# Optimization experiments

Hardware: AMD Instinct MI355X
Metric: run time of the kernel (lower is better)

Reference implementation:

```python
import jax, jax.numpy as jnp
import numpy as np

# HGT meta: 2 node types (A=0, B=1), 3 relations (src_type, dst_type)
L, T, R = 3, 2, 3
H, D = 1, 64            # PyG HGTConv default heads=1, head_dim = hidden/heads
F = H * D               # hidden_channels = input feature dim = 64
NA = NB = 131072
E = 1_000_000
REL = [(0, 1), (1, 0), (0, 0)]


def setup_inputs() -> dict:
    key = jax.random.key(0)
    ks = jax.random.split(key, 16)
    sc = 1.0 / np.sqrt(F)
    inp = {}
    inp["xA"] = jax.random.normal(ks[0], (NA, F), jnp.float32)
    inp["xB"] = jax.random.normal(ks[1], (NB, F), jnp.float32)
    # K/Q/V projections per (layer, node_type)
    inp["Wk"] = jax.random.normal(ks[2], (L, T, F, F), jnp.float32) * sc
    inp["bk"] = jnp.zeros((L, T, F), jnp.float32)
    inp["Wq"] = jax.random.normal(ks[3], (L, T, F, F), jnp.float32) * sc
    inp["bq"] = jnp.zeros((L, T, F), jnp.float32)
    inp["Wv"] = jax.random.normal(ks[4], (L, T, F, F), jnp.float32) * sc
    inp["bv"] = jnp.zeros((L, T, F), jnp.float32)
    # per (layer, relation, head) attention / message matrices and priority
    inp["a_rel"] = jax.random.normal(ks[5], (L, R, H, D, D), jnp.float32) * sc
    inp["m_rel"] = jax.random.normal(ks[6], (L, R, H, D, D), jnp.float32) * sc
    inp["p_rel"] = jnp.ones((L, R, H), jnp.float32)
    # output projection + skip gate per (layer, node_type)
    inp["Wa"] = jax.random.normal(ks[7], (L, T, F, F), jnp.float32) * sc
    inp["ba"] = jnp.zeros((L, T, F), jnp.float32)
    inp["skip"] = jnp.ones((L, T), jnp.float32)
    # final readout Linear(hidden, 1)
    inp["lin_w"] = jax.random.normal(ks[8], (F, 1), jnp.float32) * sc
    inp["lin_b"] = jnp.zeros((1,), jnp.float32)
    # edge indices: ei[0]=src, ei[1]=dst (NA == NB so one range works)
    inp["ei1"] = jax.random.randint(ks[9], (2, E), 0, NA, jnp.int32)   # A -> B
    inp["ei2"] = jax.random.randint(ks[10], (2, E), 0, NA, jnp.int32)  # B -> A
    inp["ei3"] = jax.random.randint(ks[11], (2, E), 0, NA, jnp.int32)  # A -> A
    return inp


def _hgt_layer(xs, eis, Wk, bk, Wq, bq, Wv, bv, a_rel, m_rel, p_rel, Wa, ba, skip):
    # per-type K/Q/V projections, reshaped to [N, H, D]
    k = [(xs[t] @ Wk[t] + bk[t]).reshape(-1, H, D) for t in range(T)]
    q = [(xs[t] @ Wq[t] + bq[t]).reshape(-1, H, D) for t in range(T)]
    v = [(xs[t] @ Wv[t] + bv[t]).reshape(-1, H, D) for t in range(T)]
    agg = [jnp.zeros((xs[t].shape[0], H, D), xs[t].dtype) for t in range(T)]
    inv_sqrt_d = jnp.asarray(1.0 / np.sqrt(D), xs[0].dtype)
    for r, (s, d) in enumerate(REL):
        src, dst = eis[r][0], eis[r][1]
        n_d = xs[d].shape[0]
        # relation-specific transforms on source nodes, then edge gather
        k_r = jnp.einsum('nhd,hde->nhe', k[s], a_rel[r])
        v_r = jnp.einsum('nhd,hde->nhe', v[s], m_rel[r])
        # attention score per edge per head: (q_dst . k_src) * p_rel / sqrt(D)
        score = jnp.einsum('ehd,ehd->eh', q[d][dst], k_r[src]) * p_rel[r] * inv_sqrt_d
        # segment softmax over incoming edges of each dst node (per edge type)
        mx = jax.ops.segment_max(score, dst, num_segments=n_d)
        ex = jnp.exp(score - mx[dst])
        den = jax.ops.segment_sum(ex, dst, num_segments=n_d)
        alpha = ex / den[dst]                      # [E, H]
        msg = alpha[:, :, None] * v_r[src]         # [E, H, D]
        agg[d] = agg[d] + jax.ops.segment_sum(msg, dst, num_segments=n_d)
    outs = []
    for t in range(T):
        o = jax.nn.gelu(agg[t].reshape(-1, F), approximate=False) @ Wa[t] + ba[t]
        a = jax.nn.sigmoid(skip[t])               # skip gate (out_dim == in_dim)
        outs.append(a * o + (1.0 - a) * xs[t])
    return outs


def reference(xA, xB, Wk, bk, Wq, bq, Wv, bv, a_rel, m_rel, p_rel, Wa, ba, skip,
              lin_w, lin_b, ei1, ei2, ei3):
    xs = [xA, xB]
    eis = [ei1, ei2, ei3]
    for l in range(L):
        xs = _hgt_layer(xs, eis, Wk[l], bk[l], Wq[l], bq[l], Wv[l], bv[l],
                        a_rel[l], m_rel[l], p_rel[l], Wa[l], ba[l], skip[l])
    x = jnp.concatenate(xs, axis=0)               # concat all node types
    pooled = jnp.sum(x, axis=0, keepdims=True)    # global_add_pool, batch=None
    return pooled @ lin_w + lin_b                 # Linear(hidden, 1) -> [1, 1]
```

## Files before the change

kernel.cpp:

```cpp
#include <hip/hip_runtime.h>
#include <cmath>

#define DEV __device__ __forceinline__

typedef __attribute__((ext_vector_type(8))) short short8v;
typedef __attribute__((ext_vector_type(4))) float f32x4;

DEV float atomicAddF(float* p, float v) {
    return unsafeAtomicAdd(p, v);
}

DEV float gelu_exact(float v) {
    return 0.5f * v * (1.f + erff(v * 0.70710678118654752f));
}

DEV unsigned short f32_to_bf16(float f) {
    union { float f; unsigned int u; } x; x.f = f;
    unsigned int r = x.u + 0x7fffu + ((x.u >> 16) & 1u);
    return (unsigned short)(r >> 16);
}

DEV unsigned int f4_to_fp8x4(float a, float b, float c, float d) {
    int r = __builtin_amdgcn_cvt_pk_fp8_f32(a, b, 0, false);
    r = __builtin_amdgcn_cvt_pk_fp8_f32(c, d, r, true);
    return (unsigned int)r;
}

DEV float4 fp8x4_to_f4(unsigned int w) {
    auto lo = __builtin_amdgcn_cvt_pk_f32_fp8(w, false);
    auto hi = __builtin_amdgcn_cvt_pk_f32_fp8(w, true);
    return make_float4(lo[0], lo[1], hi[0], hi[1]);
}

DEV short8v cvt8_bf16(float4 f0, float4 f1) {
    union { unsigned int u[4]; short8v s; } r;
    asm("v_cvt_pk_bf16_f32 %0, %1, %2" : "=v"(r.u[0]) : "v"(f0.x), "v"(f0.y));
    asm("v_cvt_pk_bf16_f32 %0, %1, %2" : "=v"(r.u[1]) : "v"(f0.z), "v"(f0.w));
    asm("v_cvt_pk_bf16_f32 %0, %1, %2" : "=v"(r.u[2]) : "v"(f1.x), "v"(f1.y));
    asm("v_cvt_pk_bf16_f32 %0, %1, %2" : "=v"(r.u[3]) : "v"(f1.z), "v"(f1.w));
    return r.s;
}


struct MatSetB {
    const unsigned short* Wt[3];
    const float* b[3];
    float*       y[3];
    int          mode[3];
    int          n;
};

#define BCAP2 6144
#define SB_TILE 4096
#define PSTR 129

__global__ __launch_bounds__(256) void combine_w_bf16(
    const float* __restrict__ Wk, const float* __restrict__ bk,
    const float* __restrict__ Wv, const float* __restrict__ bv,
    const float* __restrict__ a_rel, const float* __restrict__ m_rel,
    const float* __restrict__ p_rel, unsigned short* __restrict__ CWt,
    float* __restrict__ Cb)
{
    const int r = blockIdx.x, kv = blockIdx.y, l = blockIdx.z;
    const int srcT[3] = {0, 1, 0};
    const int s = srcT[r];
    const float* Wsrc = (kv == 0 ? Wk : Wv) + ((size_t)(l*2 + s)) * 4096;
    const float* bsrc = (kv == 0 ? bk : bv) + ((size_t)(l*2 + s)) * 64;
    const float* A    = (kv == 0 ? a_rel : m_rel) + ((size_t)(l*3 + r)) * 4096;
    const float scale = (kv == 0) ? p_rel[l*3 + r] * 0.125f : 1.f;

    __shared__ float Ws[4096];
    __shared__ float As[4096];
    const int tid = threadIdx.x;
    for (int k = tid; k < 4096; k += 256) { Ws[k] = Wsrc[k]; As[k] = A[k]; }
    __syncthreads();

    unsigned short* out = CWt + ((size_t)(l*6 + r*2 + kv)) * 4096;
    const int j = tid & 63;
    #pragma unroll
    for (int i = 0; i < 16; i++) {
        const int f = (tid >> 6) * 16 + i;
        float acc = 0.f;
        #pragma unroll
        for (int e = 0; e < 64; e++) acc = fmaf(Ws[f*64 + e], As[e*64 + j], acc);
        const int so = (l == 0) ? f : (4*(f & 15) + (f >> 4));
        out[j*64 + so] = f32_to_bf16(acc * scale);
    }
    if (tid < 64) {
        float acc = 0.f;
        for (int e = 0; e < 64; e++) acc = fmaf(bsrc[e], As[e*64 + tid], acc);
        Cb[(size_t)(l*6 + r*2 + kv) * 64 + tid] = acc * scale;
    }
}

__global__ __launch_bounds__(256) void prep_wt(
    const float* __restrict__ Wq, const float* __restrict__ Wa,
    unsigned short* __restrict__ Wqt, unsigned short* __restrict__ Wat)
{
    const int bid = blockIdx.x;
    const float* src; unsigned short* dst; int useSigma;
    if (bid < 6) { src = Wq + (size_t)bid * 4096; dst = Wqt + (size_t)bid * 4096;
                   useSigma = (bid >= 2); }
    else         { src = Wa + (size_t)(bid - 6) * 4096; dst = Wat + (size_t)(bid - 6) * 4096;
                   useSigma = 1; }
    for (int idx = threadIdx.x; idx < 4096; idx += 256) {
        const int c = idx >> 6, s = idx & 63;
        const int k = useSigma ? (16*(s & 3) + (s >> 2)) : s;
        dst[c*64 + s] = f32_to_bf16(src[k*64 + c]);
    }
}

__global__ __launch_bounds__(256) void proj_mfma(const float* __restrict__ x, MatSetB ms)
{
    const int tid = threadIdx.x;
    const int wv  = tid >> 6;
    const int ln  = tid & 63;
    const int j   = ln & 15;
    const int g   = ln >> 4;
    const long long rowb = (long long)blockIdx.x * 128 + wv * 32;

    short8v A[2][2];
    #pragma unroll
    for (int rg = 0; rg < 2; rg++) {
        const float* xp = x + (rowb + rg*16 + j) * 64 + g*8;
        #pragma unroll
        for (int ks = 0; ks < 2; ks++) {
            const float4 f0 = *(const float4*)(xp + ks*32);
            const float4 f1 = *(const float4*)(xp + ks*32 + 4);
            A[rg][ks] = cvt8_bf16(f0, f1);
        }
    }

    unsigned int kst[2][4];
    for (int m = 0; m < ms.n; m++) {
        short8v B[4][2];
        #pragma unroll
        for (int ct = 0; ct < 4; ct++) {
            const unsigned short* wp = ms.Wt[m] + (ct*16 + j) * 64 + g*8;
            B[ct][0] = *(const short8v*)(wp);
            B[ct][1] = *(const short8v*)(wp + 32);
        }
        f32x4 acc[2][4];
        #pragma unroll
        for (int ct = 0; ct < 4; ct++) {
            const float bm = ms.b[m][ct*16 + j];
            f32x4 bi = {bm, bm, bm, bm};
            acc[0][ct] = bi; acc[1][ct] = bi;
        }
        #pragma unroll
        for (int rg = 0; rg < 2; rg++)
            #pragma unroll
            for (int ct = 0; ct < 4; ct++) {
                acc[rg][ct] = __builtin_amdgcn_mfma_f32_16x16x32_bf16(
                    A[rg][0], B[ct][0], acc[rg][ct], 0, 0, 0);
                acc[rg][ct] = __builtin_amdgcn_mfma_f32_16x16x32_bf16(
                    A[rg][1], B[ct][1], acc[rg][ct], 0, 0, 0);
            }
        const int mode = ms.mode[m];
        if (mode == 0) {
            float* yb = ms.y[m];
            #pragma unroll
            for (int rg = 0; rg < 2; rg++)
                #pragma unroll
                for (int i = 0; i < 4; i++) {
                    const long long node = rowb + rg*16 + g*4 + i;
                    *(float4*)(yb + node*64 + j*4) = make_float4(
                        acc[rg][0][i], acc[rg][1][i], acc[rg][2][i], acc[rg][3][i]);
                }
        } else if (mode == 1) {
            #pragma unroll
            for (int rg = 0; rg < 2; rg++)
                #pragma unroll
                for (int i = 0; i < 4; i++)
                    kst[rg][i] = f4_to_fp8x4(
                        acc[rg][0][i], acc[rg][1][i], acc[rg][2][i], acc[rg][3][i]);
        } else {
            unsigned char* yb = (unsigned char*)ms.y[m];
            #pragma unroll
            for (int rg = 0; rg < 2; rg++)
                #pragma unroll
                for (int i = 0; i < 4; i++) {
                    const long long node = rowb + rg*16 + g*4 + i;
                    uint2 s;
                    s.x = kst[rg][i];
                    s.y = f4_to_fp8x4(
                        acc[rg][0][i], acc[rg][1][i], acc[rg][2][i], acc[rg][3][i]);
                    *(uint2*)(yb + node*128 + j*8) = s;
                }
        }
    }
}

__global__ __launch_bounds__(256) void scatter_bucket(
    const int* __restrict__ ei, int E, int nbuck,
    int* __restrict__ bcur, int2* __restrict__ pairbuf)
{
    __shared__ int  hist[256];
    __shared__ int  lbase[256];
    __shared__ int  gbase[256];
    __shared__ int  lcur[256];
    __shared__ int  scanbuf[256];
    __shared__ int2 stage[SB_TILE];
    const int tid = threadIdx.x;
    const int tile0 = blockIdx.x * SB_TILE;

    int2 my[16]; int mb[16];
    #pragma unroll
    for (int i = 0; i < 16; i++) {
        const int e = tile0 + tid + i*256;
        if (e < E) { my[i].x = ei[e]; my[i].y = ei[E + e]; mb[i] = my[i].y >> 9; }
        else mb[i] = -1;
    }
    hist[tid] = 0;
    __syncthreads();
    #pragma unroll
    for (int i = 0; i < 16; i++) if (mb[i] >= 0) atomicAdd(&hist[mb[i]], 1);
    __syncthreads();
    const int c = hist[tid];
    scanbuf[tid] = c;
    __syncthreads();
    for (int off = 1; off < 256; off <<= 1) {
        int add = (tid >= off) ? scanbuf[tid - off] : 0;
        __syncthreads();
        scanbuf[tid] += add;
        __syncthreads();
    }
    lbase[tid] = scanbuf[tid] - c;
    lcur[tid]  = scanbuf[tid] - c;
    if (c > 0 && tid < nbuck) gbase[tid] = atomicAdd(bcur + tid * 16, c);
    __syncthreads();
    #pragma unroll
    for (int i = 0; i < 16; i++) {
        if (mb[i] >= 0) {
            const int p = atomicAdd(&lcur[mb[i]], 1);
            stage[p] = my[i];
        }
    }
    __syncthreads();
    if (c > 0 && tid < nbuck) {
        const int gb = gbase[tid];
        const int lb = lbase[tid];
        int2* dstp = pairbuf + (size_t)tid * BCAP2;
        for (int jj = 0; jj < c; jj++) {
            const int gp = gb + jj;
            if (gp < BCAP2) dstp[gp] = stage[lb + jj];
        }
    }
}

__global__ __launch_bounds__(256) void bucket_csr(
    const int2* __restrict__ pairbuf, const int* __restrict__ bcur,
    int* __restrict__ row_ptr, int* __restrict__ row_end,
    int* __restrict__ col, int n)
{
    const int b   = blockIdx.x;
    const int tid = threadIdx.x;
    __shared__ int lcnt[512];
    __shared__ int lcur[512];
    __shared__ int scanbuf[256];
    int cnt = bcur[b * 16];
    if (cnt > BCAP2) cnt = BCAP2;
    lcnt[tid] = 0; lcnt[tid + 256] = 0;
    __syncthreads();
    const int2* src = pairbuf + (size_t)b * BCAP2;
    for (int i = tid; i < cnt; i += 256)
        atomicAdd(&lcnt[src[i].y & 511], 1);
    __syncthreads();
    const int c0 = lcnt[2*tid], c1 = lcnt[2*tid + 1];
    const int s = c0 + c1;
    scanbuf[tid] = s;
    __syncthreads();
    for (int off = 1; off < 256; off <<= 1) {
        int add = (tid >= off) ? scanbuf[tid - off] : 0;
        __syncthreads();
        scanbuf[tid] += add;
        __syncthreads();
    }
    const int excl = scanbuf[tid] - s;
    const int base = b * BCAP2;
    const int d0 = (b << 9) + 2*tid;
    if (d0 < n)     { row_ptr[d0]   = base + excl;      row_end[d0]   = base + excl + c0; }
    if (d0 + 1 < n) { row_ptr[d0+1] = base + excl + c0; row_end[d0+1] = base + excl + c0 + c1; }
    lcur[2*tid] = excl; lcur[2*tid + 1] = excl + c0;
    __syncthreads();
    for (int i = tid; i < cnt; i += 256) {
        const int2 p = src[i];
        const int pos = atomicAdd(&lcur[p.y & 511], 1);
        col[base + pos] = p.x;
    }
}

#define AGG_BODY(RP, RE, COL, KV, O0, O1)                                              \
    {                                                                                  \
        float4 acc0 = {0.f,0.f,0.f,0.f}, acc1 = {0.f,0.f,0.f,0.f};                     \
        float ssum = 0.f;                                                              \
        const int s0 = RP[dst], s1 = RE[dst];                                          \
        int src_cur = (s0 < s1) ? COL[s0] : 0;                                         \
        uint4 kvr = *(const uint4*)(KV + (size_t)src_cur * 128 + sub*16);              \
        for (int e = s0; e < s1; e++) {                                                \
            const int src_next = (e + 1 < s1) ? COL[e + 1] : 0;                        \
            const uint4 kvn = *(const uint4*)(KV + (size_t)src_next * 128 + sub*16);   \
            const float4 kA = fp8x4_to_f4(kvr.x);                                      \
            const float4 kB = fp8x4_to_f4(kvr.z);                                      \
            float sc = q0.x*kA.x + q0.y*kA.y + q0.z*kA.z + q0.w*kA.w                   \
                     + q1.x*kB.x + q1.y*kB.y + q1.z*kB.z + q1.w*kB.w;                  \
            sc += __shfl_xor(sc, 1); sc += __shfl_xor(sc, 2); sc += __shfl_xor(sc, 4); \
            const float p = __expf(sc);                                                \
            const float4 vA = fp8x4_to_f4(kvr.y);                                      \
            const float4 vB = fp8x4_to_f4(kvr.w);                                      \
            ssum += p;                                                                 \
            acc0.x = fmaf(p, vA.x, acc0.x); acc0.y = fmaf(p, vA.y, acc0.y);            \
            acc0.z = fmaf(p, vA.z, acc0.z); acc0.w = fmaf(p, vA.w, acc0.w);            \
            acc1.x = fmaf(p, vB.x, acc1.x); acc1.y = fmaf(p, vB.y, acc1.y);            \
            acc1.z = fmaf(p, vB.z, acc1.z); acc1.w = fmaf(p, vB.w, acc1.w);            \
            kvr = kvn;                                                                 \
        }                                                                              \
        const float inv = (ssum > 0.f) ? 1.f / ssum : 0.f;                             \
        O0.x = fmaf(acc0.x, inv, O0.x); O0.y = fmaf(acc0.y, inv, O0.y);                \
        O0.z = fmaf(acc0.z, inv, O0.z); O0.w = fmaf(acc0.w, inv, O0.w);                \
        O1.x = fmaf(acc1.x, inv, O1.x); O1.y = fmaf(acc1.y, inv, O1.y);                \
        O1.z = fmaf(acc1.z, inv, O1.z); O1.w = fmaf(acc1.w, inv, O1.w);                \
    }

__global__ __launch_bounds__(1024, 8) void agg_epilogue(
    const int* __restrict__ rp1, const int* __restrict__ re1, const int* __restrict__ c1,
    const int* __restrict__ rp2, const int* __restrict__ re2, const int* __restrict__ c2,
    const float* __restrict__ q,
    const unsigned char* __restrict__ kva, const unsigned char* __restrict__ kvb,
    float* __restrict__ xio, const unsigned short* __restrict__ Wat,
    const float* __restrict__ ba, const float* __restrict__ skipw,
    int xstd, int dual, int dopool, float* __restrict__ vec)
{
    __shared__ float lds[64 * PSTR];
    __shared__ float lds_pool[64];
    const int tid = threadIdx.x;
    const long long rowb = (long long)blockIdx.x * 128;
    if (tid < 64) lds_pool[tid] = 0.f;

    {
        const int sub = tid & 7;
        const int dl  = tid >> 3;
        const int dst = (int)rowb + dl;
        const float4* qp = (const float4*)(q + (size_t)dst * 64);
        const float4 q0 = qp[sub*2], q1 = qp[sub*2 + 1];
        float4 o0 = {0.f,0.f,0.f,0.f}, o1 = {0.f,0.f,0.f,0.f};
        AGG_BODY(rp1, re1, c1, kva, o0, o1)
        if (dual) {
            AGG_BODY(rp2, re2, c2, kvb, o0, o1)
        }
        float* lp = lds + (size_t)(8*sub) * PSTR + dl;
        lp[0*PSTR] = gelu_exact(o0.x); lp[1*PSTR] = gelu_exact(o0.y);
        lp[2*PSTR] = gelu_exact(o0.z); lp[3*PSTR] = gelu_exact(o0.w);
        lp[4*PSTR] = gelu_exact(o1.x); lp[5*PSTR] = gelu_exact(o1.y);
        lp[6*PSTR] = gelu_exact(o1.z); lp[7*PSTR] = gelu_exact(o1.w);
    }
    __syncthreads();

    if (tid < 512) {
        const int wv = tid >> 6;
        const int ln = tid & 63;
        const int j  = ln & 15;
        const int g  = ln >> 4;
        const int r  = wv*16 + j;

        short8v A[2];
        #pragma unroll
        for (int ks = 0; ks < 2; ks++) {
            const int pb = g*8 + ks*32;
            const float4 f0 = make_float4(lds[(pb+0)*PSTR + r], lds[(pb+1)*PSTR + r],
                                          lds[(pb+2)*PSTR + r], lds[(pb+3)*PSTR + r]);
            const float4 f1 = make_float4(lds[(pb+4)*PSTR + r], lds[(pb+5)*PSTR + r],
                                          lds[(pb+6)*PSTR + r], lds[(pb+7)*PSTR + r]);
            A[ks] = cvt8_bf16(f0, f1);
        }

        f32x4 acc[4];
        #pragma unroll
        for (int ct = 0; ct < 4; ct++) {
            const float bm = ba[ct*16 + j];
            acc[ct] = (f32x4){bm, bm, bm, bm};
        }
        #pragma unroll
        for (int ct = 0; ct < 4; ct++) {
            const unsigned short* wp = Wat + (ct*16 + j) * 64 + g*8;
            const short8v B0 = *(const short8v*)(wp);
            const short8v B1 = *(const short8v*)(wp + 32);
            acc[ct] = __builtin_amdgcn_mfma_f32_16x16x32_bf16(A[0], B0, acc[ct], 0, 0, 0);
            acc[ct] = __builtin_amdgcn_mfma_f32_16x16x32_bf16(A[1], B1, acc[ct], 0, 0, 0);
        }

        const float gate = 1.f / (1.f + __expf(-skipw[0]));
        const float og   = 1.f - gate;
        float4 pacc = {0.f,0.f,0.f,0.f};
        #pragma unroll
        for (int i = 0; i < 4; i++) {
            const long long node = rowb + wv*16 + g*4 + i;
            float* xp = xio + node*64;
            float4 o;
            if (xstd) {
                o.x = gate*acc[0][i] + og*xp[j];
                o.y = gate*acc[1][i] + og*xp[16 + j];
                o.z = gate*acc[2][i] + og*xp[32 + j];
                o.w = gate*acc[3][i] + og*xp[48 + j];
            } else {
                const float4 xo = *(const float4*)(xp + 4*j);
                o = make_float4(gate*acc[0][i] + og*xo.x,
                                gate*acc[1][i] + og*xo.y,
                                gate*acc[2][i] + og*xo.z,
                                gate*acc[3][i] + og*xo.w);
            }
            if (!dopool) {
                *(float4*)(xp + 4*j) = o;
            } else {
                pacc.x += o.x; pacc.y += o.y; pacc.z += o.z; pacc.w += o.w;
            }
        }
        if (dopool) {
            atomicAdd(&lds_pool[4*j + 0], pacc.x);
            atomicAdd(&lds_pool[4*j + 1], pacc.y);
            atomicAdd(&lds_pool[4*j + 2], pacc.z);
            atomicAdd(&lds_pool[4*j + 3], pacc.w);
        }
    }
    __syncthreads();
    if (dopool && tid < 64) atomicAddF(vec + tid, lds_pool[tid]);
}

__global__ void final_dot(const float* __restrict__ vec, const float* __restrict__ lw,
                          const float* __restrict__ lb, float* __restrict__ out)
{
    const int i = threadIdx.x;
    float v = vec[i] * lw[16*(i & 3) + (i >> 2)];
    #pragma unroll
    for (int m = 32; m >= 1; m >>= 1) v += __shfl_xor(v, m);
    if (i == 0) out[0] = v + lb[0];
}

extern "C" void kernel_launch(void* const* d_in, const int* in_sizes, int n_in,
                              void* d_out, int out_size, void* d_ws, size_t ws_size,
                              hipStream_t stream)
{
    float* xs[2] = {(float*)d_in[0], (float*)d_in[1]};
    const float* Wk    = (const float*)d_in[2];
    const float* bk    = (const float*)d_in[3];
    const float* Wq    = (const float*)d_in[4];
    const float* bq    = (const float*)d_in[5];
    const float* Wv    = (const float*)d_in[6];
    const float* bv    = (const float*)d_in[7];
    const float* a_rel = (const float*)d_in[8];
    const float* m_rel = (const float*)d_in[9];
    const float* p_rel = (const float*)d_in[10];
    const float* Wa    = (const float*)d_in[11];
    const float* ba    = (const float*)d_in[12];
    const float* skipw = (const float*)d_in[13];
    const float* lin_w = (const float*)d_in[14];
    const float* lin_b = (const float*)d_in[15];
    const int*   ei[3] = {(const int*)d_in[16], (const int*)d_in[17], (const int*)d_in[18]};

    const long long NA = in_sizes[0] / 64;
    const long long NB = in_sizes[1] / 64;
    const long long Ns[2] = {NA, NB};
    const long long Nmax = NA > NB ? NA : NB;
    int E[3];
    for (int r = 0; r < 3; r++) E[r] = in_sizes[16 + r] / 2;
    static const int dstN_is_B[3] = {1, 0, 0};
    const long long nbuckMax = (Nmax + 511) >> 9;

    float* w = (float*)d_ws;
    float* qbuf  = w; w += Nmax * 64;
    unsigned char* kv0 = (unsigned char*)w; w += Nmax * 32;
    unsigned char* kv1 = (unsigned char*)w; w += Nmax * 32;
    unsigned short* CWt = (unsigned short*)w; w += 18 * 2048;
    unsigned short* Wqt = (unsigned short*)w; w += 6 * 2048;
    unsigned short* Wat = (unsigned short*)w; w += 6 * 2048;
    float* Cb    = w; w += 18 * 64;
    float* vec   = w; w += 64;
    int* iw = (int*)w;
    int* row_ptr[3]; int* row_end[3]; int* col[3];
    for (int r = 0; r < 3; r++) {
        row_ptr[r] = iw; iw += Nmax;
        row_end[r] = iw; iw += Nmax;
        col[r]     = iw; iw += nbuckMax * BCAP2;
    }
    int*  bcur    = iw; iw += nbuckMax * 16;
    int2* pairbuf = (int2*)iw;

    combine_w_bf16<<<dim3(3, 2, 3), 256, 0, stream>>>(Wk, bk, Wv, bv, a_rel, m_rel, p_rel, CWt, Cb);
    prep_wt<<<12, 256, 0, stream>>>(Wq, Wa, Wqt, Wat);
    hipMemsetAsync(vec, 0, 64 * sizeof(float), stream);

    for (int r = 0; r < 3; r++) {
        const int n = (int)Ns[dstN_is_B[r]];
        const int nbuck = (n + 511) >> 9;
        hipMemsetAsync(bcur, 0, (size_t)nbuck * 16 * sizeof(int), stream);
        scatter_bucket<<<(E[r] + SB_TILE - 1) / SB_TILE, 256, 0, stream>>>(
            ei[r], E[r], nbuck, bcur, pairbuf);
        bucket_csr<<<nbuck, 256, 0, stream>>>(pairbuf, bcur, row_ptr[r], row_end[r], col[r], n);
    }

    const int gA = (int)(NA >> 7), gB = (int)(NB >> 7);
    for (int l = 0; l < 3; l++) {
        const int xstd   = (l == 0) ? 1 : 0;
        const int dopool = (l == 2) ? 1 : 0;
        {
            MatSetB ms; ms.n = 3;
            ms.Wt[0] = Wqt + (size_t)(l*2 + 1) * 4096;  ms.b[0] = bq + (size_t)(l*2 + 1) * 64;
            ms.y[0] = qbuf;        ms.mode[0] = 0;
            ms.Wt[1] = CWt + (size_t)(l*6 + 2) * 4096;  ms.b[1] = Cb + (size_t)(l*6 + 2) * 64;
            ms.y[1] = nullptr;     ms.mode[1] = 1;
            ms.Wt[2] = CWt + (size_t)(l*6 + 3) * 4096;  ms.b[2] = Cb + (size_t)(l*6 + 3) * 64;
            ms.y[2] = (float*)kv1; ms.mode[2] = 2;
            proj_mfma<<<gB, 256, 0, stream>>>(xs[1], ms);
        }
        {
            MatSetB ms; ms.n = 2;
            ms.Wt[0] = CWt + (size_t)(l*6 + 0) * 4096;  ms.b[0] = Cb + (size_t)(l*6 + 0) * 64;
            ms.y[0] = nullptr;     ms.mode[0] = 1;
            ms.Wt[1] = CWt + (size_t)(l*6 + 1) * 4096;  ms.b[1] = Cb + (size_t)(l*6 + 1) * 64;
            ms.y[1] = (float*)kv0; ms.mode[1] = 2;
            ms.Wt[2] = ms.Wt[1]; ms.b[2] = ms.b[1]; ms.y[2] = ms.y[1]; ms.mode[2] = 2;
            proj_mfma<<<gA, 256, 0, stream>>>(xs[0], ms);
        }
        agg_epilogue<<<gB, 1024, 0, stream>>>(
            row_ptr[0], row_end[0], col[0],
            row_ptr[0], row_end[0], col[0],
            qbuf, kv0, kv0, xs[1],
            Wat + (size_t)(l*2 + 1) * 4096, ba + (size_t)(l*2 + 1) * 64,
            skipw + l*2 + 1, xstd, 0, dopool, vec);

        {
            MatSetB ms; ms.n = 3;
            ms.Wt[0] = Wqt + (size_t)(l*2 + 0) * 4096;  ms.b[0] = bq + (size_t)(l*2 + 0) * 64;
            ms.y[0] = qbuf;        ms.mode[0] = 0;
            ms.Wt[1] = CWt + (size_t)(l*6 + 4) * 4096;  ms.b[1] = Cb + (size_t)(l*6 + 4) * 64;
            ms.y[1] = nullptr;     ms.mode[1] = 1;
            ms.Wt[2] = CWt + (size_t)(l*6 + 5) * 4096;  ms.b[2] = Cb + (size_t)(l*6 + 5) * 64;
            ms.y[2] = (float*)kv0; ms.mode[2] = 2;
            proj_mfma<<<gA, 256, 0, stream>>>(xs[0], ms);
        }
        agg_epilogue<<<gA, 1024, 0, stream>>>(
            row_ptr[1], row_end[1], col[1],
            row_ptr[2], row_end[2], col[2],
            qbuf, kv1, kv0, xs[0],
            Wat + (size_t)(l*2 + 0) * 4096, ba + (size_t)(l*2 + 0) * 64,
            skipw + l*2 + 0, xstd, 1, dopool, vec);
    }

    final_dot<<<1, 64, 0, stream>>>(vec, lin_w, lin_b, (float*)d_out);
}
```

Before: 823.0 us.

## Restructure aggregation to 4 lanes per node with wave-local epilogue tiles

The aggregation kernel now assigns 4 lanes per destination node instead of 8, and each lane handles 16 channels with two 16-byte fp8 loads per edge. The score reduction needs one fewer shuffle. Blocks shrink from 1024 to 256 threads covering 64 nodes. Each wave writes its 16 rows row-major to its own LDS tile and reads them back for its MFMA output projection, so a wave-level wait replaces the block-wide barrier, which now runs only in the pooling layer. This cuts shuffle and synchronisation overhead and gives finer-grained scheduling, at the cost of higher register pressure and fewer lanes sharing each gathered row.

After: 848.6 us. 1.03x slower.

```diff
diff --git a/kernel.cpp b/kernel.cpp
--- a/kernel.cpp
+++ b/kernel.cpp
@@ -52,7 +52,7 @@
 
 #define BCAP2 6144
 #define SB_TILE 4096
-#define PSTR 129
+#define RSTR 68
 
 __global__ __launch_bounds__(256) void combine_w_bf16(
     const float* __restrict__ Wk, const float* __restrict__ bk,
@@ -290,39 +290,57 @@
     }
 }
 
-#define AGG_BODY(RP, RE, COL, KV, O0, O1)                                              \
+#define AGG_BODY4(RP, RE, COL, KV, O0, O1, O2, O3)                                     \
     {                                                                                  \
         float4 acc0 = {0.f,0.f,0.f,0.f}, acc1 = {0.f,0.f,0.f,0.f};                     \
+        float4 acc2 = {0.f,0.f,0.f,0.f}, acc3 = {0.f,0.f,0.f,0.f};                     \
         float ssum = 0.f;                                                              \
         const int s0 = RP[dst], s1 = RE[dst];                                          \
         int src_cur = (s0 < s1) ? COL[s0] : 0;                                         \
-        uint4 kvr = *(const uint4*)(KV + (size_t)src_cur * 128 + sub*16);              \
+        const unsigned char* kvb_ = KV + sl*32;                                        \
+        uint4 c0_ = *(const uint4*)(kvb_ + (size_t)src_cur * 128);                     \
+        uint4 c1_ = *(const uint4*)(kvb_ + (size_t)src_cur * 128 + 16);                \
         for (int e = s0; e < s1; e++) {                                                \
             const int src_next = (e + 1 < s1) ? COL[e + 1] : 0;                        \
-            const uint4 kvn = *(const uint4*)(KV + (size_t)src_next * 128 + sub*16);   \
-            const float4 kA = fp8x4_to_f4(kvr.x);                                      \
-            const float4 kB = fp8x4_to_f4(kvr.z);                                      \
+            const uint4 n0_ = *(const uint4*)(kvb_ + (size_t)src_next * 128);          \
+            const uint4 n1_ = *(const uint4*)(kvb_ + (size_t)src_next * 128 + 16);     \
+            const float4 kA = fp8x4_to_f4(c0_.x);                                      \
+            const float4 kB = fp8x4_to_f4(c0_.z);                                      \
+            const float4 kC = fp8x4_to_f4(c1_.x);                                      \
+            const float4 kD = fp8x4_to_f4(c1_.z);                                      \
             float sc = q0.x*kA.x + q0.y*kA.y + q0.z*kA.z + q0.w*kA.w                   \
-                     + q1.x*kB.x + q1.y*kB.y + q1.z*kB.z + q1.w*kB.w;                  \
-            sc += __shfl_xor(sc, 1); sc += __shfl_xor(sc, 2); sc += __shfl_xor(sc, 4); \
+                     + q1.x*kB.x + q1.y*kB.y + q1.z*kB.z + q1.w*kB.w                   \
+                     + q2.x*kC.x + q2.y*kC.y + q2.z*kC.z + q2.w*kC.w                   \
+                     + q3.x*kD.x + q3.y*kD.y + q3.z*kD.z + q3.w*kD.w;                  \
+            sc += __shfl_xor(sc, 1); sc += __shfl_xor(sc, 2);                          \
             const float p = __expf(sc);                                                \
-            const float4 vA = fp8x4_to_f4(kvr.y);                                      \
-            const float4 vB = fp8x4_to_f4(kvr.w);                                      \
+            const float4 vA = fp8x4_to_f4(c0_.y);                                      \
+            const float4 vB = fp8x4_to_f4(c0_.w);                                      \
+            const float4 vC = fp8x4_to_f4(c1_.y);                                      \
+            const float4 vD = fp8x4_to_f4(c1_.w);                                      \
             ssum += p;                                                                 \
             acc0.x = fmaf(p, vA.x, acc0.x); acc0.y = fmaf(p, vA.y, acc0.y);            \
             acc0.z = fmaf(p, vA.z, acc0.z); acc0.w = fmaf(p, vA.w, acc0.w);            \
             acc1.x = fmaf(p, vB.x, acc1.x); acc1.y = fmaf(p, vB.y, acc1.y);            \
             acc1.z = fmaf(p, vB.z, acc1.z); acc1.w = fmaf(p, vB.w, acc1.w);            \
-            kvr = kvn;                                                                 \
+            acc2.x = fmaf(p, vC.x, acc2.x); acc2.y = fmaf(p, vC.y, acc2.y);            \
+            acc2.z = fmaf(p, vC.z, acc2.z); acc2.w = fmaf(p, vC.w, acc2.w);            \
+            acc3.x = fmaf(p, vD.x, acc3.x); acc3.y = fmaf(p, vD.y, acc3.y);            \
+            acc3.z = fmaf(p, vD.z, acc3.z); acc3.w = fmaf(p, vD.w, acc3.w);            \
+            c0_ = n0_; c1_ = n1_;                                                      \
         }                                                                              \
         const float inv = (ssum > 0.f) ? 1.f / ssum : 0.f;                             \
         O0.x = fmaf(acc0.x, inv, O0.x); O0.y = fmaf(acc0.y, inv, O0.y);                \
         O0.z = fmaf(acc0.z, inv, O0.z); O0.w = fmaf(acc0.w, inv, O0.w);                \
         O1.x = fmaf(acc1.x, inv, O1.x); O1.y = fmaf(acc1.y, inv, O1.y);                \
         O1.z = fmaf(acc1.z, inv, O1.z); O1.w = fmaf(acc1.w, inv, O1.w);                \
-    }
-
-__global__ __launch_bounds__(1024, 8) void agg_epilogue(
+        O2.x = fmaf(acc2.x, inv, O2.x); O2.y = fmaf(acc2.y, inv, O2.y);                \
+        O2.z = fmaf(acc2.z, inv, O2.z); O2.w = fmaf(acc2.w, inv, O2.w);                \
+        O3.x = fmaf(acc3.x, inv, O3.x); O3.y = fmaf(acc3.y, inv, O3.y);                \
+        O3.z = fmaf(acc3.z, inv, O3.z); O3.w = fmaf(acc3.w, inv, O3.w);                \
+    }
+
+__global__ __launch_bounds__(256, 6) void agg_epilogue(
     const int* __restrict__ rp1, const int* __restrict__ re1, const int* __restrict__ c1,
     const int* __restrict__ rp2, const int* __restrict__ re2, const int* __restrict__ c2,
     const float* __restrict__ q,
@@ -331,99 +349,104 @@
     const float* __restrict__ ba, const float* __restrict__ skipw,
     int xstd, int dual, int dopool, float* __restrict__ vec)
 {
-    __shared__ float lds[64 * PSTR];
+    __shared__ float ldsb[4 * 16 * RSTR];
     __shared__ float lds_pool[64];
     const int tid = threadIdx.x;
-    const long long rowb = (long long)blockIdx.x * 128;
-    if (tid < 64) lds_pool[tid] = 0.f;
+    const int w   = tid >> 6;
+    const long long rowb = (long long)blockIdx.x * 64;
+
+    if (dopool) {
+        if (tid < 64) lds_pool[tid] = 0.f;
+        __syncthreads();
+    }
 
     {
-        const int sub = tid & 7;
-        const int dl  = tid >> 3;
-        const int dst = (int)rowb + dl;
+        const int sl  = tid & 3;
+        const int gid = (tid >> 2) & 15;
+        const int dst = (int)rowb + (tid >> 2);
         const float4* qp = (const float4*)(q + (size_t)dst * 64);
-        const float4 q0 = qp[sub*2], q1 = qp[sub*2 + 1];
+        const float4 q0 = qp[sl*4], q1 = qp[sl*4+1], q2 = qp[sl*4+2], q3 = qp[sl*4+3];
         float4 o0 = {0.f,0.f,0.f,0.f}, o1 = {0.f,0.f,0.f,0.f};
-        AGG_BODY(rp1, re1, c1, kva, o0, o1)
+        float4 o2 = {0.f,0.f,0.f,0.f}, o3 = {0.f,0.f,0.f,0.f};
+        AGG_BODY4(rp1, re1, c1, kva, o0, o1, o2, o3)
         if (dual) {
-            AGG_BODY(rp2, re2, c2, kvb, o0, o1)
-        }
-        float* lp = lds + (size_t)(8*sub) * PSTR + dl;
-        lp[0*PSTR] = gelu_exact(o0.x); lp[1*PSTR] = gelu_exact(o0.y);
-        lp[2*PSTR] = gelu_exact(o0.z); lp[3*PSTR] = gelu_exact(o0.w);
-        lp[4*PSTR] = gelu_exact(o1.x); lp[5*PSTR] = gelu_exact(o1.y);
-        lp[6*PSTR] = gelu_exact(o1.z); lp[7*PSTR] = gelu_exact(o1.w);
-    }
-    __syncthreads();
-
-    if (tid < 512) {
-        const int wv = tid >> 6;
-        const int ln = tid & 63;
-        const int j  = ln & 15;
-        const int g  = ln >> 4;
-        const int r  = wv*16 + j;
-
-        short8v A[2];
-        #pragma unroll
-        for (int ks = 0; ks < 2; ks++) {
-            const int pb = g*8 + ks*32;
-            const float4 f0 = make_float4(lds[(pb+0)*PSTR + r], lds[(pb+1)*PSTR + r],
-                                          lds[(pb+2)*PSTR + r], lds[(pb+3)*PSTR + r]);
-            const float4 f1 = make_float4(lds[(pb+4)*PSTR + r], lds[(pb+5)*PSTR + r],
-                                          lds[(pb+6)*PSTR + r], lds[(pb+7)*PSTR + r]);
-            A[ks] = cvt8_bf16(f0, f1);
-        }
-
-        f32x4 acc[4];
-        #pragma unroll
-        for (int ct = 0; ct < 4; ct++) {
-            const float bm = ba[ct*16 + j];
-            acc[ct] = (f32x4){bm, bm, bm, bm};
-        }
-        #pragma unroll
-        for (int ct = 0; ct < 4; ct++) {
-            const unsigned short* wp = Wat + (ct*16 + j) * 64 + g*8;
-            const short8v B0 = *(const short8v*)(wp);
-            const short8v B1 = *(const short8v*)(wp + 32);
-            acc[ct] = __builtin_amdgcn_mfma_f32_16x16x32_bf16(A[0], B0, acc[ct], 0, 0, 0);
-            acc[ct] = __builtin_amdgcn_mfma_f32_16x16x32_bf16(A[1], B1, acc[ct], 0, 0, 0);
-        }
-
-        const float gate = 1.f / (1.f + __expf(-skipw[0]));
-        const float og   = 1.f - gate;
-        float4 pacc = {0.f,0.f,0.f,0.f};
-        #pragma unroll
-        for (int i = 0; i < 4; i++) {
-            const long long node = rowb + wv*16 + g*4 + i;
-            float* xp = xio + node*64;
-            float4 o;
-            if (xstd) {
-                o.x = gate*acc[0][i] + og*xp[j];
-                o.y = gate*acc[1][i] + og*xp[16 + j];
-                o.z = gate*acc[2][i] + og*xp[32 + j];
-                o.w = gate*acc[3][i] + og*xp[48 + j];
-            } else {
-                const float4 xo = *(const float4*)(xp + 4*j);
-                o = make_float4(gate*acc[0][i] + og*xo.x,
-                                gate*acc[1][i] + og*xo.y,
-                                gate*acc[2][i] + og*xo.z,
-                                gate*acc[3][i] + og*xo.w);
-            }
-            if (!dopool) {
-                *(float4*)(xp + 4*j) = o;
-            } else {
-                pacc.x += o.x; pacc.y += o.y; pacc.z += o.z; pacc.w += o.w;
-            }
-        }
-        if (dopool) {
-            atomicAdd(&lds_pool[4*j + 0], pacc.x);
-            atomicAdd(&lds_pool[4*j + 1], pacc.y);
-            atomicAdd(&lds_pool[4*j + 2], pacc.z);
-            atomicAdd(&lds_pool[4*j + 3], pacc.w);
-        }
-    }
-    __syncthreads();
-    if (dopool && tid < 64) atomicAddF(vec + tid, lds_pool[tid]);
+            AGG_BODY4(rp2, re2, c2, kvb, o0, o1, o2, o3)
+        }
+        float* lp = ldsb + (size_t)(w*16 + gid) * RSTR + 16*sl;
+        *(float4*)(lp)      = make_float4(gelu_exact(o0.x), gelu_exact(o0.y),
+                                          gelu_exact(o0.z), gelu_exact(o0.w));
+        *(float4*)(lp + 4)  = make_float4(gelu_exact(o1.x), gelu_exact(o1.y),
+                                          gelu_exact(o1.z), gelu_exact(o1.w));
+        *(float4*)(lp + 8)  = make_float4(gelu_exact(o2.x), gelu_exact(o2.y),
+                                          gelu_exact(o2.z), gelu_exact(o2.w));
+        *(float4*)(lp + 12) = make_float4(gelu_exact(o3.x), gelu_exact(o3.y),
+                                          gelu_exact(o3.z), gelu_exact(o3.w));
+    }
+    asm volatile("s_waitcnt lgkmcnt(0)" ::: "memory");
+    __builtin_amdgcn_sched_barrier(0);
+
+    const int ln = tid & 63;
+    const int j  = ln & 15;
+    const int g  = ln >> 4;
+    const float* lrow = ldsb + (size_t)(w*16 + j) * RSTR;
+
+    short8v A[2];
+    #pragma unroll
+    for (int ks = 0; ks < 2; ks++) {
+        const float4 f0 = *(const float4*)(lrow + g*8 + ks*32);
+        const float4 f1 = *(const float4*)(lrow + g*8 + ks*32 + 4);
+        A[ks] = cvt8_bf16(f0, f1);
+    }
+
+    f32x4 acc[4];
+    #pragma unroll
+    for (int ct = 0; ct < 4; ct++) {
+        const float bm = ba[ct*16 + j];
+        acc[ct] = (f32x4){bm, bm, bm, bm};
+    }
+    #pragma unroll
+    for (int ct = 0; ct < 4; ct++) {
+        const unsigned short* wp = Wat + (ct*16 + j) * 64 + g*8;
+        const short8v B0 = *(const short8v*)(wp);
+        const short8v B1 = *(const short8v*)(wp + 32);
+        acc[ct] = __builtin_amdgcn_mfma_f32_16x16x32_bf16(A[0], B0, acc[ct], 0, 0, 0);
+        acc[ct] = __builtin_amdgcn_mfma_f32_16x16x32_bf16(A[1], B1, acc[ct], 0, 0, 0);
+    }
+
+    const float gate = 1.f / (1.f + __expf(-skipw[0]));
+    const float og   = 1.f - gate;
+    float4 pacc = {0.f,0.f,0.f,0.f};
+    #pragma unroll
+    for (int i = 0; i < 4; i++) {
+        const long long node = rowb + w*16 + g*4 + i;
+        float* xp = xio + node*64;
+        float4 o;
+        if (xstd) {
+            o.x = gate*acc[0][i] + og*xp[j];
+            o.y = gate*acc[1][i] + og*xp[16 + j];
+            o.z = gate*acc[2][i] + og*xp[32 + j];
+            o.w = gate*acc[3][i] + og*xp[48 + j];
+        } else {
+            const float4 xo = *(const float4*)(xp + 4*j);
+            o = make_float4(gate*acc[0][i] + og*xo.x,
+                            gate*acc[1][i] + og*xo.y,
+                            gate*acc[2][i] + og*xo.z,
+                            gate*acc[3][i] + og*xo.w);
+        }
+        if (!dopool) {
+            *(float4*)(xp + 4*j) = o;
+        } else {
+            pacc.x += o.x; pacc.y += o.y; pacc.z += o.z; pacc.w += o.w;
+        }
+    }
+    if (dopool) {
+        atomicAdd(&lds_pool[4*j + 0], pacc.x);
+        atomicAdd(&lds_pool[4*j + 1], pacc.y);
+        atomicAdd(&lds_pool[4*j + 2], pacc.z);
+        atomicAdd(&lds_pool[4*j + 3], pacc.w);
+        __syncthreads();
+        if (tid < 64) atomicAddF(vec + tid, lds_pool[tid]);
+    }
 }
 
 __global__ void final_dot(const float* __restrict__ vec, const float* __restrict__ lw,
@@ -499,6 +522,7 @@
     }
 
     const int gA = (int)(NA >> 7), gB = (int)(NB >> 7);
+    const int aA = (int)(NA >> 6), aB = (int)(NB >> 6);
     for (int l = 0; l < 3; l++) {
         const int xstd   = (l == 0) ? 1 : 0;
         const int dopool = (l == 2) ? 1 : 0;
@@ -521,7 +545,7 @@
             ms.Wt[2] = ms.Wt[1]; ms.b[2] = ms.b[1]; ms.y[2] = ms.y[1]; ms.mode[2] = 2;
             proj_mfma<<<gA, 256, 0, stream>>>(xs[0], ms);
         }
-        agg_epilogue<<<gB, 1024, 0, stream>>>(
+        agg_epilogue<<<aB, 256, 0, stream>>>(
             row_ptr[0], row_end[0], col[0],
             row_ptr[0], row_end[0], col[0],
             qbuf, kv0, kv0, xs[1],
@@ -538,7 +562,7 @@
             ms.y[2] = (float*)kv0; ms.mode[2] = 2;
             proj_mfma<<<gA, 256, 0, stream>>>(xs[0], ms);
         }
-        agg_epilogue<<<gA, 1024, 0, stream>>>(
+        agg_epilogue<<<aA, 256, 0, stream>>>(
             row_ptr[1], row_end[1], col[1],
             row_ptr[2], row_end[2], col[2],
             qbuf, kv1, kv0, xs[0],
```

## Sort destinations by degree within tiles and unroll edge loop by two

Applied to the files above, without the earlier changes.

Adds a tile_perm kernel that ranks the 128 destination nodes of each tile by in-degree and stores a per-tile permutation. The aggregation kernel uses it so that the 8 destinations sharing a 64-lane wavefront have similar degrees, which cuts divergence where lanes wait on the longest row. The edge loop is also unrolled by two, with two gathers prefetched per step to raise memory-level parallelism. This costs an extra preprocessing pass, an extra indirection load per thread, and higher register pressure.

After: 857.5 us. +4.2%, slower.

```diff
diff --git a/kernel.cpp b/kernel.cpp
--- a/kernel.cpp
+++ b/kernel.cpp
@@ -290,36 +290,72 @@
     }
 }
 
+__global__ __launch_bounds__(128) void tile_perm(
+    const int* __restrict__ rp1, const int* __restrict__ re1,
+    const int* __restrict__ rp2, const int* __restrict__ re2,
+    int dual, int n, unsigned char* __restrict__ perm)
+{
+    const int t   = threadIdx.x;
+    const int dst = blockIdx.x * 128 + t;
+    int deg = 0;
+    if (dst < n) {
+        deg = re1[dst] - rp1[dst];
+        if (dual) deg += re2[dst] - rp2[dst];
+    }
+    __shared__ int degs[128];
+    degs[t] = deg;
+    __syncthreads();
+    int rank = 0;
+    for (int i = 0; i < 128; i++) {
+        const int di = degs[i];
+        rank += (di > deg) || (di == deg && i < t);
+    }
+    perm[(size_t)blockIdx.x * 128 + rank] = (unsigned char)t;
+}
+
+#define PROC_EDGE(KVR)                                                                 \
+    {                                                                                  \
+        const float4 ka_ = fp8x4_to_f4(KVR.x);                                         \
+        const float4 kb2_ = fp8x4_to_f4(KVR.z);                                        \
+        float sc_ = q0.x*ka_.x + q0.y*ka_.y + q0.z*ka_.z + q0.w*ka_.w                  \
+                  + q1.x*kb2_.x + q1.y*kb2_.y + q1.z*kb2_.z + q1.w*kb2_.w;             \
+        sc_ += __shfl_xor(sc_, 1); sc_ += __shfl_xor(sc_, 2); sc_ += __shfl_xor(sc_, 4);\
+        const float p_ = __expf(sc_);                                                  \
+        const float4 va_ = fp8x4_to_f4(KVR.y);                                         \
+        const float4 vb_ = fp8x4_to_f4(KVR.w);                                         \
+        ssum_ += p_;                                                                   \
+        acc0_.x = fmaf(p_, va_.x, acc0_.x); acc0_.y = fmaf(p_, va_.y, acc0_.y);        \
+        acc0_.z = fmaf(p_, va_.z, acc0_.z); acc0_.w = fmaf(p_, va_.w, acc0_.w);        \
+        acc1_.x = fmaf(p_, vb_.x, acc1_.x); acc1_.y = fmaf(p_, vb_.y, acc1_.y);        \
+        acc1_.z = fmaf(p_, vb_.z, acc1_.z); acc1_.w = fmaf(p_, vb_.w, acc1_.w);        \
+    }
+
 #define AGG_BODY(RP, RE, COL, KV, O0, O1)                                              \
     {                                                                                  \
-        float4 acc0 = {0.f,0.f,0.f,0.f}, acc1 = {0.f,0.f,0.f,0.f};                     \
-        float ssum = 0.f;                                                              \
-        const int s0 = RP[dst], s1 = RE[dst];                                          \
-        int src_cur = (s0 < s1) ? COL[s0] : 0;                                         \
-        uint4 kvr = *(const uint4*)(KV + (size_t)src_cur * 128 + sub*16);              \
-        for (int e = s0; e < s1; e++) {                                                \
-            const int src_next = (e + 1 < s1) ? COL[e + 1] : 0;                        \
-            const uint4 kvn = *(const uint4*)(KV + (size_t)src_next * 128 + sub*16);   \
-            const float4 kA = fp8x4_to_f4(kvr.x);                                      \
-            const float4 kB = fp8x4_to_f4(kvr.z);                                      \
-            float sc = q0.x*kA.x + q0.y*kA.y + q0.z*kA.z + q0.w*kA.w                   \
-                     + q1.x*kB.x + q1.y*kB.y + q1.z*kB.z + q1.w*kB.w;                  \
-            sc += __shfl_xor(sc, 1); sc += __shfl_xor(sc, 2); sc += __shfl_xor(sc, 4); \
-            const float p = __expf(sc);                                                \
-            const float4 vA = fp8x4_to_f4(kvr.y);                                      \
-            const float4 vB = fp8x4_to_f4(kvr.w);                                      \
-            ssum += p;                                                                 \
-            acc0.x = fmaf(p, vA.x, acc0.x); acc0.y = fmaf(p, vA.y, acc0.y);            \
-            acc0.z = fmaf(p, vA.z, acc0.z); acc0.w = fmaf(p, vA.w, acc0.w);            \
-            acc1.x = fmaf(p, vB.x, acc1.x); acc1.y = fmaf(p, vB.y, acc1.y);            \
-            acc1.z = fmaf(p, vB.z, acc1.z); acc1.w = fmaf(p, vB.w, acc1.w);            \
-            kvr = kvn;                                                                 \
+        float4 acc0_ = {0.f,0.f,0.f,0.f}, acc1_ = {0.f,0.f,0.f,0.f};                   \
+        float ssum_ = 0.f;                                                             \
+        const int ss0_ = (RP)[dst], ss1_ = (RE)[dst];                                  \
+        const unsigned char* kb_ = (KV) + sub*16;                                      \
+        int e_ = ss0_;                                                                 \
+        uint4 cc0_ = {0,0,0,0}, cc1_ = {0,0,0,0};                                      \
+        if (e_ < ss1_)     cc0_ = *(const uint4*)(kb_ + (size_t)(COL)[e_] * 128);      \
+        if (e_ + 1 < ss1_) cc1_ = *(const uint4*)(kb_ + (size_t)(COL)[e_+1] * 128);    \
+        for (; e_ + 2 < ss1_; e_ += 2) {                                               \
+            const int nn0_ = (COL)[e_+2];                                              \
+            const int nn1_ = (e_ + 3 < ss1_) ? (COL)[e_+3] : nn0_;                     \
+            const uint4 pp0_ = *(const uint4*)(kb_ + (size_t)nn0_ * 128);              \
+            const uint4 pp1_ = *(const uint4*)(kb_ + (size_t)nn1_ * 128);              \
+            PROC_EDGE(cc0_)                                                            \
+            PROC_EDGE(cc1_)                                                            \
+            cc0_ = pp0_; cc1_ = pp1_;                                                  \
         }                                                                              \
-        const float inv = (ssum > 0.f) ? 1.f / ssum : 0.f;                             \
-        O0.x = fmaf(acc0.x, inv, O0.x); O0.y = fmaf(acc0.y, inv, O0.y);                \
-        O0.z = fmaf(acc0.z, inv, O0.z); O0.w = fmaf(acc0.w, inv, O0.w);                \
-        O1.x = fmaf(acc1.x, inv, O1.x); O1.y = fmaf(acc1.y, inv, O1.y);                \
-        O1.z = fmaf(acc1.z, inv, O1.z); O1.w = fmaf(acc1.w, inv, O1.w);                \
+        if (e_ < ss1_)     PROC_EDGE(cc0_)                                             \
+        if (e_ + 1 < ss1_) PROC_EDGE(cc1_)                                             \
+        const float inv_ = (ssum_ > 0.f) ? 1.f / ssum_ : 0.f;                          \
+        O0.x = fmaf(acc0_.x, inv_, O0.x); O0.y = fmaf(acc0_.y, inv_, O0.y);            \
+        O0.z = fmaf(acc0_.z, inv_, O0.z); O0.w = fmaf(acc0_.w, inv_, O0.w);            \
+        O1.x = fmaf(acc1_.x, inv_, O1.x); O1.y = fmaf(acc1_.y, inv_, O1.y);            \
+        O1.z = fmaf(acc1_.z, inv_, O1.z); O1.w = fmaf(acc1_.w, inv_, O1.w);            \
     }
 
 __global__ __launch_bounds__(1024, 8) void agg_epilogue(
@@ -327,6 +363,7 @@
     const int* __restrict__ rp2, const int* __restrict__ re2, const int* __restrict__ c2,
     const float* __restrict__ q,
     const unsigned char* __restrict__ kva, const unsigned char* __restrict__ kvb,
+    const unsigned char* __restrict__ perm,
     float* __restrict__ xio, const unsigned short* __restrict__ Wat,
     const float* __restrict__ ba, const float* __restrict__ skipw,
     int xstd, int dual, int dopool, float* __restrict__ vec)
@@ -339,7 +376,7 @@
 
     {
         const int sub = tid & 7;
-        const int dl  = tid >> 3;
+        const int dl  = perm[(size_t)blockIdx.x * 128 + (tid >> 3)];
         const int dst = (int)rowb + dl;
         const float4* qp = (const float4*)(q + (size_t)dst * 64);
         const float4 q0 = qp[sub*2], q1 = qp[sub*2 + 1];
@@ -475,6 +512,8 @@
     unsigned short* Wat = (unsigned short*)w; w += 6 * 2048;
     float* Cb    = w; w += 18 * 64;
     float* vec   = w; w += 64;
+    unsigned char* permB = (unsigned char*)w; w += Nmax / 4;
+    unsigned char* permA = (unsigned char*)w; w += Nmax / 4;
     int* iw = (int*)w;
     int* row_ptr[3]; int* row_end[3]; int* col[3];
     for (int r = 0; r < 3; r++) {
@@ -497,6 +536,10 @@
             ei[r], E[r], nbuck, bcur, pairbuf);
         bucket_csr<<<nbuck, 256, 0, stream>>>(pairbuf, bcur, row_ptr[r], row_end[r], col[r], n);
     }
+    tile_perm<<<(int)((NB + 127) / 128), 128, 0, stream>>>(
+        row_ptr[0], row_end[0], row_ptr[0], row_end[0], 0, (int)NB, permB);
+    tile_perm<<<(int)((NA + 127) / 128), 128, 0, stream>>>(
+        row_ptr[1], row_end[1], row_ptr[2], row_end[2], 1, (int)NA, permA);
 
     const int gA = (int)(NA >> 7), gB = (int)(NB >> 7);
     for (int l = 0; l < 3; l++) {
@@ -524,7 +567,7 @@
         agg_epilogue<<<gB, 1024, 0, stream>>>(
             row_ptr[0], row_end[0], col[0],
             row_ptr[0], row_end[0], col[0],
-            qbuf, kv0, kv0, xs[1],
+            qbuf, kv0, kv0, permB, xs[1],
             Wat + (size_t)(l*2 + 1) * 4096, ba + (size_t)(l*2 + 1) * 64,
             skipw + l*2 + 1, xstd, 0, dopool, vec);
 
@@ -541,7 +584,7 @@
         agg_epilogue<<<gA, 1024, 0, stream>>>(
             row_ptr[1], row_end[1], col[1],
             row_ptr[2], row_end[2], col[2],
-            qbuf, kv1, kv0, xs[0],
+            qbuf, kv1, kv0, permA, xs[0],
             Wat + (size_t)(l*2 + 0) * 4096, ba + (size_t)(l*2 + 0) * 64,
             skipw + l*2 + 0, xstd, 1, dopool, vec);
     }
```
